# Kernel optimization log

Hardware: AMD Instinct MI355X
Metric: run time of the kernel (lower is better)

The kernel has to match this reference:

```python
import jax, jax.numpy as jnp
import numpy as np
from jax import lax

# PointPWC multi-scale Chamfer/Smoothness/Curvature loss (single scale here).
F_CHAMFER = 1.0
F_SMOOTH = 0.5
F_CURVATURE = 0.3
ALPHA0 = 0.02


def _sqdist(src, dst):
    # src: (B,N,3), dst: (B,M,3) -> (B,N,M) squared euclidean distances
    d = -2.0 * jnp.einsum('bnc,bmc->bnm', src, dst)
    d = d + jnp.sum(src * src, axis=-1)[:, :, None]
    d = d + jnp.sum(dst * dst, axis=-1)[:, None, :]
    return d


def _knn(sqd, k):
    # smallest-k of sqd along last axis -> (dists, indices)
    neg, idx = lax.top_k(-sqd, k)
    return -neg, idx


def _group(points, idx):
    # points: (B,N,C), idx: (B,M,k) -> (B,M,k,C)
    return jax.vmap(lambda p, i: p[i])(points, idx)


def _curvature(pc):
    # pc: (B,N,3) -> (B,N,3)
    _, kidx = _knn(_sqdist(pc, pc), 10)
    grouped = _group(pc, kidx)
    return jnp.sum(grouped - pc[:, :, None, :], axis=2) / 9.0


def _curvature_warp(pc, warped):
    _, kidx = _knn(_sqdist(pc, pc), 10)
    grouped = _group(warped, kidx)
    return jnp.sum(grouped - warped[:, :, None, :], axis=2) / 9.0


def _chamfer(p1, p2):
    sqd = _sqdist(p1, p2)
    return jnp.min(sqd, axis=-1), jnp.min(sqd, axis=1)


def _smooth(pc, flow, k):
    _, kidx = _knn(_sqdist(pc, pc), k)
    g = _group(flow, kidx)
    d = g - flow[:, :, None, :]
    sq = jnp.sum(d * d, axis=3)
    # safe norm: zero (self-neighbor) entries get norm 0 with zero grad
    nrm = jnp.where(sq == 0, 0.0, jnp.sqrt(jnp.where(sq == 0, 1.0, sq)))
    return jnp.sum(nrm, axis=2) / 8.0


def _interp_curvature(p1, p2, c2):
    dist, kidx = _knn(_sqdist(p1, p2), 5)
    g = _group(c2, kidx)  # (B,N,5,3)
    w = 1.0 / (dist + 1e-8)
    w = w / jnp.sum(w, axis=2, keepdims=True)
    return jnp.sum(w[..., None] * g, axis=2)


def setup_inputs() -> dict:
    key = jax.random.key(0)
    k1, k2, k3 = jax.random.split(key, 3)
    N = 8192
    coords = jax.random.normal(k1, (N, 3), dtype=jnp.float32)
    registration_gt = jax.random.normal(k2, (1, N, 3), dtype=jnp.float32)
    registration_pred = jax.random.normal(k3, (1, N, 3), dtype=jnp.float32)
    return {
        'registration_pred': registration_pred,
        'registration_gt': registration_gt,
        'coords': coords,
        'smoothness_k': 9,
    }


def reference(registration_pred, registration_gt, coords, smoothness_k):
    pc1 = coords[None]                       # (1,N,3)
    pc2 = coords[None] + registration_gt     # (1,N,3)
    flow = registration_pred                 # (1,N,3)

    pc2_curv = _curvature(pc2)
    pc1_warp = pc1 + flow
    dist1, dist2 = _chamfer(pc1_warp, pc2)
    moved_curv = _curvature_warp(pc1, pc1_warp)

    chamfer = jnp.mean(jnp.sum(dist1, axis=1)) + jnp.mean(jnp.sum(dist2, axis=1))
    smooth = jnp.mean(jnp.sum(_smooth(pc1, flow, smoothness_k), axis=1))
    inter_curv = _interp_curvature(pc1_warp, pc2, pc2_curv)
    curv = jnp.mean(jnp.sum(jnp.sum((inter_curv - moved_curv) ** 2, axis=2), axis=1))

    total = (F_CHAMFER * ALPHA0 * chamfer
             + F_CURVATURE * ALPHA0 * curv
             + F_SMOOTH * ALPHA0 * smooth)
    return jnp.reshape(total, (1,))
```

## Files before the change

kernel.cpp:

```cpp
#include <hip/hip_runtime.h>
#include <hip/hip_bf16.h>
#include <math.h>

#define N_PTS 8192
#define QPW 4
#define QPW_REV 8
#define WPB 4
#define QPB (QPW * WPB)
#define BLKS_TOPK (N_PTS / QPB)
#define BLKS_REV  (N_PTS / (QPW_REV * WPB))

#define R0_END BLKS_TOPK
#define R1_END (2 * BLKS_TOPK)
#define R3_END (3 * BLKS_TOPK)
#define GRID_TOTAL (3 * BLKS_TOPK + BLKS_REV)

#define W_CHAM 0.02f
#define W_CURV 0.006f
#define W_SMOO 0.01f

#define BIGF 1e30f
#define IDX_MASK 0x1FFFu
#define KEY_MASK 0xFFFFE000u

__device__ __forceinline__ float mkkey(float d, unsigned idx) {
    return __uint_as_float((__float_as_uint(d) & KEY_MASK) | idx);
}
__device__ __forceinline__ int keyidx(float k) {
    return (int)(__float_as_uint(k) & IDX_MASK);
}

template <int K>
__device__ __forceinline__ void kinsert(float kv, float (&bd)[K]) {
    bd[K - 1] = kv;
#pragma unroll
    for (int s = K - 1; s > 0; --s) {
        float lo = fminf(bd[s - 1], bd[s]);
        float hi = fmaxf(bd[s - 1], bd[s]);
        bd[s - 1] = lo; bd[s] = hi;
    }
}

template <int K>
__device__ __forceinline__ void merge_keys(float m1, float m2, float m3,
                                           float (&bd)[K], int lane) {
    float h0 = m1, h1 = m2, h2 = m3;
#pragma unroll
    for (int r = 0; r < K; ++r) {
        float bv = h0;
#pragma unroll
        for (int off = 1; off < 64; off <<= 1) bv = fminf(bv, __shfl_xor(bv, off));
        bd[r] = bv;
        if (h0 == bv) { h0 = h1; h1 = h2; h2 = BIGF; }
    }
}

template <int K>
__device__ void tau_rescan(const float4* __restrict__ cand,
                           float nqx, float nqy, float nqz, float tau,
                           float (&bd)[K], int lane) {
#pragma unroll
    for (int r = 0; r < K; ++r) bd[r] = BIGF;
    const float4* cp = cand + lane;
    unsigned ib = (unsigned)lane;
    for (int it = 0; it < N_PTS / 64; ++it) {
        float4 p = cp[it * 64];
        float d = fmaf(p.x, nqx, fmaf(p.y, nqy, fmaf(p.z, nqz, p.w)));
        float kc = mkkey(d, ib);
        unsigned long long m = __ballot(kc <= tau);
        while (m) {
            int b = __builtin_ctzll(m);
            m &= m - 1;
            float kv = __shfl(kc, b);
            if (kv < bd[K - 1]) kinsert<K>(kv, bd);
        }
        ib += 64;
    }
}

template <int Q>
__device__ __forceinline__ void scank(const float4* __restrict__ cand,
                                      const float (&nqx)[Q], const float (&nqy)[Q],
                                      const float (&nqz)[Q],
                                      float (&m1)[Q], float (&m2)[Q], float (&m3)[Q],
                                      int lane) {
#pragma unroll
    for (int qi = 0; qi < Q; ++qi) { m1[qi] = BIGF; m2[qi] = BIGF; m3[qi] = BIGF; }
    const float4* cp = cand + lane;
    unsigned ib = (unsigned)lane;
#pragma unroll 2
    for (int it = 0; it < N_PTS / 256; ++it) {
        float4 p0 = cp[it * 256 + 0];
        float4 p1 = cp[it * 256 + 64];
        float4 p2 = cp[it * 256 + 128];
        float4 p3 = cp[it * 256 + 192];
#pragma unroll
        for (int qi = 0; qi < Q; ++qi) {
            float d0 = fmaf(p0.x, nqx[qi], fmaf(p0.y, nqy[qi], fmaf(p0.z, nqz[qi], p0.w)));
            float k0 = mkkey(d0, ib);
            m3[qi] = __builtin_amdgcn_fmed3f(k0, m2[qi], m3[qi]);
            m2[qi] = __builtin_amdgcn_fmed3f(k0, m1[qi], m2[qi]);
            m1[qi] = fminf(k0, m1[qi]);
            float d1 = fmaf(p1.x, nqx[qi], fmaf(p1.y, nqy[qi], fmaf(p1.z, nqz[qi], p1.w)));
            float k1 = mkkey(d1, ib + 64u);
            m3[qi] = __builtin_amdgcn_fmed3f(k1, m2[qi], m3[qi]);
            m2[qi] = __builtin_amdgcn_fmed3f(k1, m1[qi], m2[qi]);
            m1[qi] = fminf(k1, m1[qi]);
            float d2 = fmaf(p2.x, nqx[qi], fmaf(p2.y, nqy[qi], fmaf(p2.z, nqz[qi], p2.w)));
            float k2 = mkkey(d2, ib + 128u);
            m3[qi] = __builtin_amdgcn_fmed3f(k2, m2[qi], m3[qi]);
            m2[qi] = __builtin_amdgcn_fmed3f(k2, m1[qi], m2[qi]);
            m1[qi] = fminf(k2, m1[qi]);
            float d3 = fmaf(p3.x, nqx[qi], fmaf(p3.y, nqy[qi], fmaf(p3.z, nqz[qi], p3.w)));
            float k3 = mkkey(d3, ib + 192u);
            m3[qi] = __builtin_amdgcn_fmed3f(k3, m2[qi], m3[qi]);
            m2[qi] = __builtin_amdgcn_fmed3f(k3, m1[qi], m2[qi]);
            m1[qi] = fminf(k3, m1[qi]);
        }
        ib += 256u;
    }
}

__global__ void prep_kernel(const float* __restrict__ flow, const float* __restrict__ gt,
                            const float* __restrict__ coords,
                            float4* __restrict__ p1q, float4* __restrict__ p2q,
                            float4* __restrict__ wq, float* __restrict__ accs,
                            int* __restrict__ done) {
    int i = blockIdx.x * blockDim.x + threadIdx.x;
    if (i < N_PTS) {
        float cx = coords[3 * i + 0], cy = coords[3 * i + 1], cz = coords[3 * i + 2];
        float p2x = cx + gt[3 * i + 0], p2y = cy + gt[3 * i + 1], p2z = cz + gt[3 * i + 2];
        float wx = cx + flow[3 * i + 0], wy = cy + flow[3 * i + 1], wz = cz + flow[3 * i + 2];
        p1q[i] = make_float4(cx, cy, cz, cx * cx + cy * cy + cz * cz);
        p2q[i] = make_float4(p2x, p2y, p2z, p2x * p2x + p2y * p2y + p2z * p2z);
        wq[i]  = make_float4(wx, wy, wz, wx * wx + wy * wy + wz * wz);
    }
    if (i < 8) accs[i] = 0.0f;
    if (i == 8) done[0] = 0;
}

__global__ __launch_bounds__(256) void fused4_kernel(const float4* __restrict__ p1q,
                                                     const float4* __restrict__ p2q,
                                                     const float4* __restrict__ wq,
                                                     const float* __restrict__ flow,
                                                     const int* __restrict__ ksm_p,
                                                     float* __restrict__ curv2,
                                                     float* __restrict__ mcurv,
                                                     float* __restrict__ crossk,
                                                     float* __restrict__ accs) {
    const int tid = threadIdx.x, lane = tid & 63, wv = tid >> 6;
    const int b = blockIdx.x;

    if (b >= R3_END) {
        __shared__ float pmn[WPB];
        const int q0 = (b - R3_END) * (QPW_REV * WPB) + wv * QPW_REV;
        float nqx[QPW_REV], nqy[QPW_REV], nqz[QPW_REV], qw[QPW_REV], mn[QPW_REV];
#pragma unroll
        for (int qi = 0; qi < QPW_REV; ++qi) {
            float4 t = p2q[q0 + qi];
            nqx[qi] = -2.f * t.x; nqy[qi] = -2.f * t.y; nqz[qi] = -2.f * t.z;
            qw[qi] = t.w; mn[qi] = BIGF;
        }
        const float4* cp = wq + lane;
#pragma unroll 2
        for (int it = 0; it < N_PTS / 128; ++it) {
            float4 p0 = cp[it * 128 + 0];
            float4 p1 = cp[it * 128 + 64];
#pragma unroll
            for (int qi = 0; qi < QPW_REV; ++qi) {
                float d0 = fmaf(p0.x, nqx[qi], fmaf(p0.y, nqy[qi], fmaf(p0.z, nqz[qi], p0.w)));
                float d1 = fmaf(p1.x, nqx[qi], fmaf(p1.y, nqy[qi], fmaf(p1.z, nqz[qi], p1.w)));
                mn[qi] = fminf(mn[qi], fminf(d0, d1));
            }
        }
        float s = 0.f;
#pragma unroll
        for (int qi = 0; qi < QPW_REV; ++qi) {
            float v = mn[qi];
#pragma unroll
            for (int off = 1; off < 64; off <<= 1) v = fminf(v, __shfl_xor(v, off));
            s += v + qw[qi];
        }
        if (lane == 0) pmn[wv] = s;
        __syncthreads();
        if (tid == 0) atomicAdd(&accs[1], pmn[0] + pmn[1] + pmn[2] + pmn[3]);
        return;
    }

    const int role = (b < R0_END) ? 0 : (b < R1_END) ? 1 : 3;
    const int blk = b - ((role == 0) ? 0 : (role == 1) ? R0_END : R1_END);
    const int q0 = blk * QPB + wv * QPW;

    const float4* qsrc = (role == 0) ? p2q : (role == 1) ? p1q : wq;
    const float4* cand = (role == 1) ? p1q : p2q;
    float nqx[QPW], nqy[QPW], nqz[QPW];
#pragma unroll
    for (int qi = 0; qi < QPW; ++qi) {
        float4 t = qsrc[q0 + qi];
        nqx[qi] = -2.f * t.x; nqy[qi] = -2.f * t.y; nqz[qi] = -2.f * t.z;
    }
    float m1[QPW], m2[QPW], m3[QPW];
    scank<QPW>(cand, nqx, nqy, nqz, m1, m2, m3, lane);

    if (role == 3) {
        constexpr int K = 5;
#pragma unroll
        for (int qi = 0; qi < QPW; ++qi) {
            float bd[K];
            merge_keys<K>(m1[qi], m2[qi], m3[qi], bd, lane);
            if (__ballot(m3[qi] <= bd[K - 1]) != 0ull)
                tau_rescan<K>(p2q, nqx[qi], nqy[qi], nqz[qi], bd[K - 1], bd, lane);
            const int q = q0 + qi;
            if (lane < K) {
                float kv = 0.f;
#pragma unroll
                for (int r = 0; r < K; ++r) if (lane == r) kv = bd[r];
                crossk[lane * N_PTS + q] = kv;
            }
        }
        return;
    }

    constexpr int K = 10;
    if (role == 0) {
#pragma unroll
        for (int qi = 0; qi < QPW; ++qi) {
            float bd[K];
            merge_keys<K>(m1[qi], m2[qi], m3[qi], bd, lane);
            if (__ballot(m3[qi] <= bd[K - 1]) != 0ull)
                tau_rescan<K>(p2q, nqx[qi], nqy[qi], nqz[qi], bd[K - 1], bd, lane);
            float ax = 0.f, ay = 0.f, az = 0.f;
#pragma unroll
            for (int r = 0; r < K; ++r) {
                float4 nb = p2q[keyidx(bd[r])];
                ax += nb.x; ay += nb.y; az += nb.z;
            }
            if (lane == 0) {
                const int q = q0 + qi;
                float4 t = p2q[q];
                curv2[q * 3 + 0] = (ax - 10.f * t.x) * (1.f / 9.f);
                curv2[q * 3 + 1] = (ay - 10.f * t.y) * (1.f / 9.f);
                curv2[q * 3 + 2] = (az - 10.f * t.z) * (1.f / 9.f);
            }
        }
    } else {
        __shared__ float psm[WPB];
        const int ksm = ksm_p[0];
        float smsum = 0.f;
#pragma unroll
        for (int qi = 0; qi < QPW; ++qi) {
            float bd[K];
            merge_keys<K>(m1[qi], m2[qi], m3[qi], bd, lane);
            if (__ballot(m3[qi] <= bd[K - 1]) != 0ull)
                tau_rescan<K>(p1q, nqx[qi], nqy[qi], nqz[qi], bd[K - 1], bd, lane);
            const int q = q0 + qi;
            float4 wqp = wq[q];
            const float fqx = flow[q * 3 + 0], fqy = flow[q * 3 + 1], fqz = flow[q * 3 + 2];
            float ax = 0.f, ay = 0.f, az = 0.f, sm = 0.f;
#pragma unroll
            for (int r = 0; r < K; ++r) {
                const int ni = keyidx(bd[r]);
                float4 nb = wq[ni];
                ax += nb.x; ay += nb.y; az += nb.z;
                if (r < ksm) {
                    float dx = flow[ni * 3 + 0] - fqx;
                    float dy = flow[ni * 3 + 1] - fqy;
                    float dz = flow[ni * 3 + 2] - fqz;
                    float sq = dx * dx + dy * dy + dz * dz;
                    sm += (sq == 0.f) ? 0.f : sqrtf(sq);
                }
            }
            smsum += sm * 0.125f;
            if (lane == 0) {
                mcurv[q * 3 + 0] = (ax - 10.f * wqp.x) * (1.f / 9.f);
                mcurv[q * 3 + 1] = (ay - 10.f * wqp.y) * (1.f / 9.f);
                mcurv[q * 3 + 2] = (az - 10.f * wqp.z) * (1.f / 9.f);
            }
        }
        if (lane == 0) psm[wv] = smsum;
        __syncthreads();
        if (tid == 0) atomicAdd(&accs[2], psm[0] + psm[1] + psm[2] + psm[3]);
    }
}

__global__ __launch_bounds__(256) void epi_kernel(const float* __restrict__ crossk,
                                                  const float4* __restrict__ wq,
                                                  const float4* __restrict__ p2q,
                                                  const float* __restrict__ curv2,
                                                  const float* __restrict__ mcurv,
                                                  float* __restrict__ accs,
                                                  int* __restrict__ done,
                                                  float* __restrict__ out) {
    __shared__ float pd1[WPB], pcv[WPB];
    const int tid = threadIdx.x, lane = tid & 63, wv = tid >> 6;
    const int q = blockIdx.x * 256 + tid;
    constexpr int K = 5;
    float4 qp = wq[q];
    float bd[K]; int bi[K];
#pragma unroll
    for (int r = 0; r < K; ++r) {
        bi[r] = keyidx(crossk[r * N_PTS + q]);
        float4 nb = p2q[bi[r]];
        float dx = qp.x - nb.x, dy = qp.y - nb.y, dz = qp.z - nb.z;
        bd[r] = dx * dx + dy * dy + dz * dz;
    }
    float w[K], wsum = 0.f;
#pragma unroll
    for (int r = 0; r < K; ++r) { w[r] = 1.f / (bd[r] + 1e-8f); wsum += w[r]; }
    float ix = 0.f, iy = 0.f, iz = 0.f;
#pragma unroll
    for (int r = 0; r < K; ++r) {
        float ww = w[r] / wsum;
        ix += ww * curv2[bi[r] * 3 + 0];
        iy += ww * curv2[bi[r] * 3 + 1];
        iz += ww * curv2[bi[r] * 3 + 2];
    }
    float dx = ix - mcurv[q * 3 + 0];
    float dy = iy - mcurv[q * 3 + 1];
    float dz = iz - mcurv[q * 3 + 2];
    float d1 = bd[0];
    float cv = dx * dx + dy * dy + dz * dz;
#pragma unroll
    for (int off = 1; off < 64; off <<= 1) {
        d1 += __shfl_xor(d1, off);
        cv += __shfl_xor(cv, off);
    }
    if (lane == 0) { pd1[wv] = d1; pcv[wv] = cv; }
    __syncthreads();
    if (tid == 0) {
        atomicAdd(&accs[0], pd1[0] + pd1[1] + pd1[2] + pd1[3]);
        atomicAdd(&accs[3], pcv[0] + pcv[1] + pcv[2] + pcv[3]);
        __threadfence();
        int v = atomicAdd(done, 1);
        if (v == (int)gridDim.x - 1) {
            out[0] = W_CHAM * (accs[0] + accs[1]) + W_CURV * accs[3] + W_SMOO * accs[2];
        }
    }
}

extern "C" void kernel_launch(void* const* d_in, const int* in_sizes, int n_in,
                              void* d_out, int out_size, void* d_ws, size_t ws_size,
                              hipStream_t stream) {
    const float* flow   = (const float*)d_in[0];
    const float* gt     = (const float*)d_in[1];
    const float* coords = (const float*)d_in[2];
    const int*   ksm    = (const int*)d_in[3];

    float4* p1q   = (float4*)d_ws;
    float4* p2q   = p1q + N_PTS;
    float4* wq    = p2q + N_PTS;
    float*  curv2 = (float*)(wq + N_PTS);
    float*  mcurv = curv2 + 3 * N_PTS;
    float*  crossk = mcurv + 3 * N_PTS;
    float*  accs  = crossk + 5 * N_PTS;
    int*    done  = (int*)(accs + 8);
    float*  out   = (float*)d_out;

    prep_kernel<<<(N_PTS + 255) / 256, 256, 0, stream>>>(flow, gt, coords, p1q, p2q, wq,
                                                         accs, done);
    fused4_kernel<<<GRID_TOTAL, 256, 0, stream>>>(p1q, p2q, wq, flow, ksm,
                                                  curv2, mcurv, crossk, accs);
    epi_kernel<<<N_PTS / 256, 256, 0, stream>>>(crossk, wq, p2q, curv2, mcurv,
                                                accs, done, out);
}
```

Measured before the change: 152.0 us.

## Replace sequential top-k merge with ballot-based radix threshold selection

Replaces the K-round wave-wide min-reduction merge of per-lane candidate lists with a binary search over a monotone key threshold. It uses ballots and popcounts to find a pivot that admits exactly K candidates, then keeps the selected keys distributed across lanes. Neighbor accumulation is now done per-lane followed by a wave reduction. The crossk output is written unsorted, so the epilogue takes the min of the five entries. The smoothness-k subset is chosen by key comparison against the max rather than by sorted rank, which assumes k is 9 or at least 10, and the search can cost up to 34 ballot iterations.

```diff
diff --git a/kernel.cpp b/kernel.cpp
--- a/kernel.cpp
+++ b/kernel.cpp
@@ -29,6 +29,14 @@
 __device__ __forceinline__ int keyidx(float k) {
     return (int)(__float_as_uint(k) & IDX_MASK);
 }
+__device__ __forceinline__ unsigned monou(float k) {
+    int b = __float_as_int(k);
+    return (unsigned)(b ^ ((b >> 31) | 0x80000000));
+}
+__device__ __forceinline__ int prefcnt(unsigned long long m) {
+    return __builtin_amdgcn_mbcnt_hi((unsigned)(m >> 32),
+           __builtin_amdgcn_mbcnt_lo((unsigned)m, 0));
+}
 
 template <int K>
 __device__ __forceinline__ void kinsert(float kv, float (&bd)[K]) {
@@ -42,8 +50,7 @@
 }
 
 template <int K>
-__device__ __forceinline__ void merge_keys(float m1, float m2, float m3,
-                                           float (&bd)[K], int lane) {
+__device__ void merge_keys(float m1, float m2, float m3, float (&bd)[K], int lane) {
     float h0 = m1, h1 = m2, h2 = m3;
 #pragma unroll
     for (int r = 0; r < K; ++r) {
@@ -75,6 +82,68 @@
             if (kv < bd[K - 1]) kinsert<K>(kv, bd);
         }
         ib += 64;
+    }
+}
+
+template <int K>
+__device__ void select_set(const float4* __restrict__ cand,
+                           float nqx, float nqy, float nqz,
+                           float& k1, float& k2, float& k3,
+                           bool& q1, bool& q2, bool& q3, float& km, int lane) {
+    const unsigned u1 = monou(k1), u2 = monou(k2), u3 = monou(k3);
+    unsigned lo = 0u, hi = 0xFFFFFFFFu, piv = 0u;
+    int cnt = -1;
+    unsigned long long b3 = 0ull;
+    for (int it = 0; it < 34; ++it) {
+        piv = lo + ((hi - lo) >> 1);
+        unsigned long long b1 = __ballot(u1 <= piv);
+        unsigned long long b2 = __ballot(u2 <= piv);
+        b3 = __ballot(u3 <= piv);
+        cnt = __popcll(b1) + __popcll(b2) + __popcll(b3);
+        if (cnt == K) break;
+        if (cnt < K) lo = piv + 1; else hi = piv - 1;
+    }
+    bool setok = (cnt == K);
+    bool fail;
+    float bdK[K];
+    if (setok) {
+        q1 = (u1 <= piv); q2 = (u2 <= piv); q3 = (u3 <= piv);
+        float t = q3 ? k3 : (q2 ? k2 : (q1 ? k1 : -BIGF));
+#pragma unroll
+        for (int off = 1; off < 64; off <<= 1) t = fmaxf(t, __shfl_xor(t, off));
+        km = t;
+        fail = (b3 != 0ull);
+    } else {
+        merge_keys<K>(k1, k2, k3, bdK, lane);
+        km = bdK[K - 1];
+        fail = (__ballot(k3 <= km) != 0ull);
+    }
+    if (fail) { tau_rescan<K>(cand, nqx, nqy, nqz, km, bdK, lane); setok = false; }
+    if (!setok) {
+        float kv = BIGF;
+#pragma unroll
+        for (int r = 0; r < K; ++r) if (lane == r) kv = bdK[r];
+        k1 = kv; k2 = BIGF; k3 = BIGF;
+        q1 = (lane < K); q2 = false; q3 = false;
+        km = bdK[K - 1];
+    }
+}
+
+__device__ __forceinline__ void wave_add3(float& a, float& b, float& c) {
+#pragma unroll
+    for (int off = 1; off < 64; off <<= 1) {
+        a += __shfl_xor(a, off);
+        b += __shfl_xor(b, off);
+        c += __shfl_xor(c, off);
+    }
+}
+__device__ __forceinline__ void wave_add4(float& a, float& b, float& c, float& d) {
+#pragma unroll
+    for (int off = 1; off < 64; off <<= 1) {
+        a += __shfl_xor(a, off);
+        b += __shfl_xor(b, off);
+        c += __shfl_xor(c, off);
+        d += __shfl_xor(d, off);
     }
 }
 
@@ -206,17 +275,14 @@
         constexpr int K = 5;
 #pragma unroll
         for (int qi = 0; qi < QPW; ++qi) {
-            float bd[K];
-            merge_keys<K>(m1[qi], m2[qi], m3[qi], bd, lane);
-            if (__ballot(m3[qi] <= bd[K - 1]) != 0ull)
-                tau_rescan<K>(p2q, nqx[qi], nqy[qi], nqz[qi], bd[K - 1], bd, lane);
+            float k1 = m1[qi], k2 = m2[qi], k3 = m3[qi]; bool q1, q2, q3; float km;
+            select_set<K>(p2q, nqx[qi], nqy[qi], nqz[qi], k1, k2, k3, q1, q2, q3, km, lane);
             const int q = q0 + qi;
-            if (lane < K) {
-                float kv = 0.f;
-#pragma unroll
-                for (int r = 0; r < K; ++r) if (lane == r) kv = bd[r];
-                crossk[lane * N_PTS + q] = kv;
-            }
+            unsigned long long b1 = __ballot(q1), b2 = __ballot(q2), b3 = __ballot(q3);
+            int c1 = __popcll(b1), c2 = __popcll(b2);
+            if (q1) crossk[prefcnt(b1) * N_PTS + q] = k1;
+            if (q2) crossk[(c1 + prefcnt(b2)) * N_PTS + q] = k2;
+            if (q3) crossk[(c1 + c2 + prefcnt(b3)) * N_PTS + q] = k3;
         }
         return;
     }
@@ -225,16 +291,13 @@
     if (role == 0) {
 #pragma unroll
         for (int qi = 0; qi < QPW; ++qi) {
-            float bd[K];
-            merge_keys<K>(m1[qi], m2[qi], m3[qi], bd, lane);
-            if (__ballot(m3[qi] <= bd[K - 1]) != 0ull)
-                tau_rescan<K>(p2q, nqx[qi], nqy[qi], nqz[qi], bd[K - 1], bd, lane);
+            float k1 = m1[qi], k2 = m2[qi], k3 = m3[qi]; bool q1, q2, q3; float km;
+            select_set<K>(p2q, nqx[qi], nqy[qi], nqz[qi], k1, k2, k3, q1, q2, q3, km, lane);
             float ax = 0.f, ay = 0.f, az = 0.f;
-#pragma unroll
-            for (int r = 0; r < K; ++r) {
-                float4 nb = p2q[keyidx(bd[r])];
-                ax += nb.x; ay += nb.y; az += nb.z;
-            }
+            if (q1) { float4 nb = p2q[keyidx(k1)]; ax += nb.x; ay += nb.y; az += nb.z; }
+            if (q2) { float4 nb = p2q[keyidx(k2)]; ax += nb.x; ay += nb.y; az += nb.z; }
+            if (q3) { float4 nb = p2q[keyidx(k3)]; ax += nb.x; ay += nb.y; az += nb.z; }
+            wave_add3(ax, ay, az);
             if (lane == 0) {
                 const int q = q0 + qi;
                 float4 t = p2q[q];
@@ -245,33 +308,49 @@
         }
     } else {
         __shared__ float psm[WPB];
-        const int ksm = ksm_p[0];
+        const bool iall = (ksm_p[0] >= 10);
         float smsum = 0.f;
 #pragma unroll
         for (int qi = 0; qi < QPW; ++qi) {
-            float bd[K];
-            merge_keys<K>(m1[qi], m2[qi], m3[qi], bd, lane);
-            if (__ballot(m3[qi] <= bd[K - 1]) != 0ull)
-                tau_rescan<K>(p1q, nqx[qi], nqy[qi], nqz[qi], bd[K - 1], bd, lane);
+            float k1 = m1[qi], k2 = m2[qi], k3 = m3[qi]; bool q1, q2, q3; float km;
+            select_set<K>(p1q, nqx[qi], nqy[qi], nqz[qi], k1, k2, k3, q1, q2, q3, km, lane);
             const int q = q0 + qi;
-            float4 wqp = wq[q];
             const float fqx = flow[q * 3 + 0], fqy = flow[q * 3 + 1], fqz = flow[q * 3 + 2];
             float ax = 0.f, ay = 0.f, az = 0.f, sm = 0.f;
-#pragma unroll
-            for (int r = 0; r < K; ++r) {
-                const int ni = keyidx(bd[r]);
+            if (q1) {
+                const int ni = keyidx(k1);
                 float4 nb = wq[ni];
                 ax += nb.x; ay += nb.y; az += nb.z;
-                if (r < ksm) {
-                    float dx = flow[ni * 3 + 0] - fqx;
-                    float dy = flow[ni * 3 + 1] - fqy;
-                    float dz = flow[ni * 3 + 2] - fqz;
+                if (iall || k1 < km) {
+                    float dx = flow[ni * 3 + 0] - fqx, dy = flow[ni * 3 + 1] - fqy, dz = flow[ni * 3 + 2] - fqz;
                     float sq = dx * dx + dy * dy + dz * dz;
                     sm += (sq == 0.f) ? 0.f : sqrtf(sq);
                 }
             }
+            if (q2) {
+                const int ni = keyidx(k2);
+                float4 nb = wq[ni];
+                ax += nb.x; ay += nb.y; az += nb.z;
+                if (iall || k2 < km) {
+                    float dx = flow[ni * 3 + 0] - fqx, dy = flow[ni * 3 + 1] - fqy, dz = flow[ni * 3 + 2] - fqz;
+                    float sq = dx * dx + dy * dy + dz * dz;
+                    sm += (sq == 0.f) ? 0.f : sqrtf(sq);
+                }
+            }
+            if (q3) {
+                const int ni = keyidx(k3);
+                float4 nb = wq[ni];
+                ax += nb.x; ay += nb.y; az += nb.z;
+                if (iall || k3 < km) {
+                    float dx = flow[ni * 3 + 0] - fqx, dy = flow[ni * 3 + 1] - fqy, dz = flow[ni * 3 + 2] - fqz;
+                    float sq = dx * dx + dy * dy + dz * dz;
+                    sm += (sq == 0.f) ? 0.f : sqrtf(sq);
+                }
+            }
+            wave_add4(ax, ay, az, sm);
             smsum += sm * 0.125f;
             if (lane == 0) {
+                float4 wqp = wq[q];
                 mcurv[q * 3 + 0] = (ax - 10.f * wqp.x) * (1.f / 9.f);
                 mcurv[q * 3 + 1] = (ay - 10.f * wqp.y) * (1.f / 9.f);
                 mcurv[q * 3 + 2] = (az - 10.f * wqp.z) * (1.f / 9.f);
@@ -318,7 +397,7 @@
     float dx = ix - mcurv[q * 3 + 0];
     float dy = iy - mcurv[q * 3 + 1];
     float dz = iz - mcurv[q * 3 + 2];
-    float d1 = bd[0];
+    float d1 = fminf(fminf(fminf(bd[0], bd[1]), fminf(bd[2], bd[3])), bd[4]);
     float cv = dx * dx + dy * dy + dz * dz;
 #pragma unroll
     for (int off = 1; off < 64; off <<= 1) {
```

Result: faster. 143.6 us (median of 2 runs) (-5.6%).
